# Kernel optimization log

Hardware: AMD Instinct MI355X
Metric: run time of the kernel (lower is better)

## Reference

```python
import jax, jax.numpy as jnp
import numpy as np

N_NODES = 100000
N_EDGES = 3200000
N_GRAPHS = 32
D_IN = 128
D_HID = 128
N_CLASSES = 10


def setup_inputs() -> dict:
    key = jax.random.key(0)
    ks = jax.random.split(key, 16)
    h = jax.random.normal(ks[0], (N_NODES, D_IN), dtype=jnp.float32)
    src = jax.random.randint(ks[1], (N_EDGES,), 0, N_NODES, dtype=jnp.int32)
    dst = jax.random.randint(ks[2], (N_EDGES,), 0, N_NODES, dtype=jnp.int32)
    graph_ids = jnp.sort(jax.random.randint(ks[3], (N_NODES,), 0, N_GRAPHS, dtype=jnp.int32))
    def lin(k, fi, fo):
        s = 1.0 / np.sqrt(fi)
        kw, kb = jax.random.split(k)
        W = jax.random.uniform(kw, (fi, fo), minval=-s, maxval=s, dtype=jnp.float32)
        b = jax.random.uniform(kb, (fo,), minval=-s, maxval=s, dtype=jnp.float32)
        return W, b
    W1, b1 = lin(ks[4], D_IN, D_HID)
    W2, b2 = lin(ks[5], D_HID, D_HID)
    W3, b3 = lin(ks[6], D_HID, D_HID)
    W4, b4 = lin(ks[7], D_HID, D_HID)
    Wc1, bc1 = lin(ks[8], D_HID, D_HID)
    Wc2, bc2 = lin(ks[9], D_HID, N_CLASSES)
    return {"h": h, "src": src, "dst": dst, "graph_ids": graph_ids,
            "W1": W1, "b1": b1, "W2": W2, "b2": b2, "W3": W3, "b3": b3,
            "W4": W4, "b4": b4, "Wc1": Wc1, "bc1": bc1, "Wc2": Wc2, "bc2": bc2}


def _graph_conv(h, src, dst, inv_sqrt_out, inv_sqrt_in, W, b):
    # DGL GraphConv, norm='both': D_dst^{-1/2} A D_src^{-1/2} h W + b
    m = (h * inv_sqrt_out[:, None])[src]            # [E, D] gathered messages
    agg = jax.ops.segment_sum(m, dst, num_segments=h.shape[0])  # [N, D]
    return (agg * inv_sqrt_in[:, None]) @ W + b


def reference(h, src, dst, graph_ids, W1, b1, W2, b2, W3, b3, W4, b4, Wc1, bc1, Wc2, bc2):
    n = h.shape[0]
    ones_e = jnp.ones(src.shape[0], dtype=jnp.float32)
    out_deg = jnp.clip(jax.ops.segment_sum(ones_e, src, num_segments=n), 1.0)
    in_deg = jnp.clip(jax.ops.segment_sum(ones_e, dst, num_segments=n), 1.0)
    inv_sqrt_out = jax.lax.rsqrt(out_deg)
    inv_sqrt_in = jax.lax.rsqrt(in_deg)

    x = jax.nn.relu(_graph_conv(h, src, dst, inv_sqrt_out, inv_sqrt_in, W1, b1))
    x = jax.nn.relu(_graph_conv(x, src, dst, inv_sqrt_out, inv_sqrt_in, W2, b2))
    x = jax.nn.relu(_graph_conv(x, src, dst, inv_sqrt_out, inv_sqrt_in, W3, b3))
    x = jax.nn.relu(_graph_conv(x, src, dst, inv_sqrt_out, inv_sqrt_in, W4, b4))

    # dgl.mean_nodes over batched graphs
    sums = jax.ops.segment_sum(x, graph_ids, num_segments=N_GRAPHS)     # [G, D]
    counts = jax.ops.segment_sum(jnp.ones(n, dtype=jnp.float32), graph_ids, num_segments=N_GRAPHS)
    hg = sums / jnp.clip(counts, 1.0)[:, None]

    out = jax.nn.relu(hg @ Wc1 + bc1)
    out = out @ Wc2 + bc2
    return out
```

## Files before the change

### kernel.cpp

```cpp
#include <hip/hip_runtime.h>

#define D 128
#define NG 32
#define NC 10

typedef unsigned short ushort_t;

__device__ __forceinline__ ushort_t f2bf(float x) {
  union { float f; unsigned u; } v; v.f = x;
  unsigned r = (v.u + 0x7FFF + ((v.u >> 16) & 1)) >> 16;
  return (ushort_t)r;
}
__device__ __forceinline__ float bf2f(ushort_t b) {
  union { unsigned u; float f; } v; v.u = ((unsigned)b) << 16;
  return v.f;
}

__global__ void degree_kernel(const int* __restrict__ src, const int* __restrict__ dst,
                              int* __restrict__ cout_, int* __restrict__ cursor,
                              int* __restrict__ rank, int E) {
  int i = blockIdx.x * 256 + threadIdx.x;
  int e0 = i * 4;
  if (e0 + 4 <= E) {
    int4 s = *(const int4*)(src + e0);
    int4 d_ = *(const int4*)(dst + e0);
    int r0 = atomicAdd(&cursor[d_.x], 1);
    int r1 = atomicAdd(&cursor[d_.y], 1);
    int r2 = atomicAdd(&cursor[d_.z], 1);
    int r3 = atomicAdd(&cursor[d_.w], 1);
    atomicAdd(&cout_[s.x], 1);
    atomicAdd(&cout_[s.y], 1);
    atomicAdd(&cout_[s.z], 1);
    atomicAdd(&cout_[s.w], 1);
    *(int4*)(rank + e0) = make_int4(r0, r1, r2, r3);
  } else {
    for (int e = e0; e < E; ++e) {
      rank[e] = atomicAdd(&cursor[dst[e]], 1);
      atomicAdd(&cout_[src[e]], 1);
    }
  }
}

__global__ void scan1_kernel(const int* __restrict__ cnt, int* __restrict__ bsum, int n) {
  __shared__ int sdata[256];
  int base = blockIdx.x * 1024 + threadIdx.x * 4;
  int s = 0;
#pragma unroll
  for (int j = 0; j < 4; ++j) {
    int idx = base + j;
    if (idx < n) s += cnt[idx];
  }
  sdata[threadIdx.x] = s;
  __syncthreads();
  for (int off = 128; off > 0; off >>= 1) {
    if (threadIdx.x < off) sdata[threadIdx.x] += sdata[threadIdx.x + off];
    __syncthreads();
  }
  if (threadIdx.x == 0) bsum[blockIdx.x] = sdata[0];
}

__global__ void scan2_kernel(int* __restrict__ bsum, int nb) {
  if (blockIdx.x == 0 && threadIdx.x == 0) {
    int acc = 0;
    for (int i = 0; i < nb; ++i) { int v = bsum[i]; bsum[i] = acc; acc += v; }
  }
}

__global__ void scan3_kernel(const int* __restrict__ cnt, const int* __restrict__ bsum,
                             int* __restrict__ rowptr, int n, int e_total) {
  __shared__ int ss[256];
  int t = threadIdx.x;
  int idx0 = blockIdx.x * 1024 + t * 4;
  int v[4]; int ts = 0;
#pragma unroll
  for (int j = 0; j < 4; ++j) {
    v[j] = (idx0 + j < n) ? cnt[idx0 + j] : 0;
    ts += v[j];
  }
  ss[t] = ts;
  __syncthreads();
  for (int off = 1; off < 256; off <<= 1) {
    int add = 0;
    if (t >= off) add = ss[t - off];
    __syncthreads();
    if (t >= off) ss[t] += add;
    __syncthreads();
  }
  int excl = ss[t] - ts + bsum[blockIdx.x];
#pragma unroll
  for (int j = 0; j < 4; ++j) {
    int idx = idx0 + j;
    if (idx < n) rowptr[idx] = excl;
    excl += v[j];
  }
  if (blockIdx.x == 0 && t == 0) rowptr[n] = e_total;
}

__global__ void passB_kernel(const int* __restrict__ src, const int* __restrict__ dst,
                             const int* __restrict__ rank, const int* __restrict__ rowptr,
                             int* __restrict__ csrc, int E) {
  int i = blockIdx.x * 256 + threadIdx.x;
  int e0 = i * 4;
  if (e0 + 4 <= E) {
    int4 s = *(const int4*)(src + e0);
    int4 d_ = *(const int4*)(dst + e0);
    int4 r = *(const int4*)(rank + e0);
    csrc[rowptr[d_.x] + r.x] = s.x;
    csrc[rowptr[d_.y] + r.y] = s.y;
    csrc[rowptr[d_.z] + r.z] = s.z;
    csrc[rowptr[d_.w] + r.w] = s.w;
  } else {
    for (int e = e0; e < E; ++e)
      csrc[rowptr[dst[e]] + rank[e]] = src[e];
  }
}

__global__ __launch_bounds__(256) void gemm_f32in_kernel(const float* __restrict__ A,
    const float* __restrict__ W, const int* __restrict__ cout_,
    ushort_t* __restrict__ X, int n) {
  __shared__ float As[64][132];
  int row0 = blockIdx.x * 64;
  for (int i = threadIdx.x; i < 64 * 32; i += 256) {
    int r = i >> 5, c4 = (i & 31) * 4;
    int row = row0 + r;
    float4 v = make_float4(0.f, 0.f, 0.f, 0.f);
    if (row < n) v = *(const float4*)(A + (size_t)row * D + c4);
    *(float4*)&As[r][c4] = v;
  }
  __syncthreads();
  int cg = threadIdx.x & 31, rg = threadIdx.x >> 5;
  int col = cg * 4;
  float4 acc[8];
#pragma unroll
  for (int r = 0; r < 8; ++r) acc[r] = make_float4(0.f, 0.f, 0.f, 0.f);
  for (int k = 0; k < D; k += 4) {
    float4 w0 = *(const float4*)(W + (size_t)k * D + col);
    float4 w1 = *(const float4*)(W + (size_t)(k + 1) * D + col);
    float4 w2 = *(const float4*)(W + (size_t)(k + 2) * D + col);
    float4 w3 = *(const float4*)(W + (size_t)(k + 3) * D + col);
#pragma unroll
    for (int r = 0; r < 8; ++r) {
      float4 a = *(const float4*)&As[rg * 8 + r][k];
      acc[r].x += a.x * w0.x + a.y * w1.x + a.z * w2.x + a.w * w3.x;
      acc[r].y += a.x * w0.y + a.y * w1.y + a.z * w2.y + a.w * w3.y;
      acc[r].z += a.x * w0.z + a.y * w1.z + a.z * w2.z + a.w * w3.z;
      acc[r].w += a.x * w0.w + a.y * w1.w + a.z * w2.w + a.w * w3.w;
    }
  }
#pragma unroll
  for (int r = 0; r < 8; ++r) {
    int row = row0 + rg * 8 + r;
    if (row < n) {
      float sc = rsqrtf(fmaxf((float)cout_[row], 1.f));
      ushort_t o[4] = { f2bf(acc[r].x * sc), f2bf(acc[r].y * sc),
                        f2bf(acc[r].z * sc), f2bf(acc[r].w * sc) };
      *(uint2*)(X + (size_t)row * D + col) = *(const uint2*)o;
    }
  }
}

__global__ __launch_bounds__(256) void gemm_bf16in_kernel(const ushort_t* __restrict__ A,
    const float* __restrict__ W, const int* __restrict__ cout_,
    ushort_t* __restrict__ X, int n) {
  __shared__ float As[64][132];
  int row0 = blockIdx.x * 64;
  for (int i = threadIdx.x; i < 64 * 32; i += 256) {
    int r = i >> 5, c4 = (i & 31) * 4;
    int row = row0 + r;
    float4 v = make_float4(0.f, 0.f, 0.f, 0.f);
    if (row < n) {
      ushort4 u = *(const ushort4*)(A + (size_t)row * D + c4);
      v.x = bf2f(u.x); v.y = bf2f(u.y); v.z = bf2f(u.z); v.w = bf2f(u.w);
    }
    *(float4*)&As[r][c4] = v;
  }
  __syncthreads();
  int cg = threadIdx.x & 31, rg = threadIdx.x >> 5;
  int col = cg * 4;
  float4 acc[8];
#pragma unroll
  for (int r = 0; r < 8; ++r) acc[r] = make_float4(0.f, 0.f, 0.f, 0.f);
  for (int k = 0; k < D; k += 4) {
    float4 w0 = *(const float4*)(W + (size_t)k * D + col);
    float4 w1 = *(const float4*)(W + (size_t)(k + 1) * D + col);
    float4 w2 = *(const float4*)(W + (size_t)(k + 2) * D + col);
    float4 w3 = *(const float4*)(W + (size_t)(k + 3) * D + col);
#pragma unroll
    for (int r = 0; r < 8; ++r) {
      float4 a = *(const float4*)&As[rg * 8 + r][k];
      acc[r].x += a.x * w0.x + a.y * w1.x + a.z * w2.x + a.w * w3.x;
      acc[r].y += a.x * w0.y + a.y * w1.y + a.z * w2.y + a.w * w3.y;
      acc[r].z += a.x * w0.z + a.y * w1.z + a.z * w2.z + a.w * w3.z;
      acc[r].w += a.x * w0.w + a.y * w1.w + a.z * w2.w + a.w * w3.w;
    }
  }
#pragma unroll
  for (int r = 0; r < 8; ++r) {
    int row = row0 + rg * 8 + r;
    if (row < n) {
      float sc = rsqrtf(fmaxf((float)cout_[row], 1.f));
      ushort_t o[4] = { f2bf(acc[r].x * sc), f2bf(acc[r].y * sc),
                        f2bf(acc[r].z * sc), f2bf(acc[r].w * sc) };
      *(uint2*)(X + (size_t)row * D + col) = *(const uint2*)o;
    }
  }
}

__global__ __launch_bounds__(256) void agg_relu_kernel(const ushort_t* __restrict__ x,
    const int* __restrict__ rowptr, const int* __restrict__ csrc,
    const int* __restrict__ cin_, const float* __restrict__ bias,
    ushort_t* __restrict__ y, int n) {
  int node = blockIdx.x * 4 + (threadIdx.x >> 6);
  if (node >= n) return;
  int lane = threadIdx.x & 63;
  int beg = rowptr[node], end = rowptr[node + 1];
  float ax = 0.f, ay = 0.f;
  const ushort_t* xp = x + (size_t)(lane * 2);
  int e = beg;
  for (; e + 8 <= end; e += 8) {
    int s[8];
#pragma unroll
    for (int j = 0; j < 8; ++j) s[j] = csrc[e + j];
    ushort2 u[8];
#pragma unroll
    for (int j = 0; j < 8; ++j) u[j] = *(const ushort2*)(xp + (size_t)s[j] * D);
#pragma unroll
    for (int j = 0; j < 8; ++j) { ax += bf2f(u[j].x); ay += bf2f(u[j].y); }
  }
  if (e + 4 <= end) {
    int s[4];
#pragma unroll
    for (int j = 0; j < 4; ++j) s[j] = csrc[e + j];
    ushort2 u[4];
#pragma unroll
    for (int j = 0; j < 4; ++j) u[j] = *(const ushort2*)(xp + (size_t)s[j] * D);
#pragma unroll
    for (int j = 0; j < 4; ++j) { ax += bf2f(u[j].x); ay += bf2f(u[j].y); }
    e += 4;
  }
  for (; e < end; ++e) {
    int s = csrc[e];
    ushort2 u = *(const ushort2*)(xp + (size_t)s * D);
    ax += bf2f(u.x); ay += bf2f(u.y);
  }
  float wi = rsqrtf(fmaxf((float)cin_[node], 1.f));
  float2 bb = *(const float2*)(bias + lane * 2);
  ushort_t o[2] = { f2bf(fmaxf(ax * wi + bb.x, 0.f)), f2bf(fmaxf(ay * wi + bb.y, 0.f)) };
  *(unsigned*)(y + (size_t)node * D + lane * 2) = *(const unsigned*)o;
}

__device__ int lower_bound_gid(const int* gid, int n, int g) {
  int lo = 0, hi = n;
  while (lo < hi) { int mid = (lo + hi) >> 1; if (gid[mid] < g) lo = mid + 1; else hi = mid; }
  return lo;
}

__global__ void pool_kernel(const ushort_t* __restrict__ x, const int* __restrict__ gid,
                            float* __restrict__ sums, int* __restrict__ counts, int n) {
  int g = blockIdx.x >> 3, part = blockIdx.x & 7;
  __shared__ int s_lo, s_hi;
  if (threadIdx.x == 0) {
    s_lo = lower_bound_gid(gid, n, g);
    s_hi = lower_bound_gid(gid, n, g + 1);
    if (part == 0) counts[g] = s_hi - s_lo;
  }
  __syncthreads();
  int lo = s_lo, hi = s_hi;
  int cnt = hi - lo;
  int per = (cnt + 7) >> 3;
  int a = lo + part * per;
  int bnd = min(a + per, hi);
  int t = threadIdx.x;
  float acc = 0.f;
  for (int i = a; i < bnd; ++i) acc += bf2f(x[(size_t)i * D + t]);
  atomicAdd(&sums[g * D + t], acc);
}

__global__ __launch_bounds__(128) void classifier_kernel(const float* __restrict__ sums,
    const int* __restrict__ counts, const float* __restrict__ Wc1, const float* __restrict__ bc1,
    const float* __restrict__ Wc2, const float* __restrict__ bc2, float* __restrict__ out) {
  __shared__ float hg[NG][D];
  __shared__ float hid[NG][D];
  int t = threadIdx.x;
#pragma unroll
  for (int g = 0; g < NG; ++g)
    hg[g][t] = sums[g * D + t] / fmaxf((float)counts[g], 1.f);
  __syncthreads();
  float acc[NG];
#pragma unroll
  for (int g = 0; g < NG; ++g) acc[g] = bc1[t];
  for (int k = 0; k < D; ++k) {
    float w = Wc1[k * D + t];
#pragma unroll
    for (int g = 0; g < NG; ++g) acc[g] += hg[g][k] * w;
  }
#pragma unroll
  for (int g = 0; g < NG; ++g) hid[g][t] = fmaxf(acc[g], 0.f);
  __syncthreads();
  for (int idx = t; idx < NG * NC; idx += 128) {
    int g = idx / NC, c = idx % NC;
    float a = bc2[c];
    for (int j = 0; j < D; ++j) a += hid[g][j] * Wc2[j * NC + c];
    out[idx] = a;
  }
}

extern "C" void kernel_launch(void* const* d_in, const int* in_sizes, int n_in,
                              void* d_out, int out_size, void* d_ws, size_t ws_size,
                              hipStream_t stream) {
  const float* h   = (const float*)d_in[0];
  const int* src   = (const int*)d_in[1];
  const int* dst   = (const int*)d_in[2];
  const int* gid   = (const int*)d_in[3];
  const float* W1  = (const float*)d_in[4];
  const float* b1  = (const float*)d_in[5];
  const float* W2  = (const float*)d_in[6];
  const float* b2  = (const float*)d_in[7];
  const float* W3  = (const float*)d_in[8];
  const float* b3  = (const float*)d_in[9];
  const float* W4  = (const float*)d_in[10];
  const float* b4  = (const float*)d_in[11];
  const float* Wc1 = (const float*)d_in[12];
  const float* bc1 = (const float*)d_in[13];
  const float* Wc2 = (const float*)d_in[14];
  const float* bc2 = (const float*)d_in[15];
  float* out = (float*)d_out;

  const int N = in_sizes[3];
  const int E = in_sizes[1];

  char* ws = (char*)d_ws;
  size_t off = 0;
  auto alloc = [&](size_t bytes) -> char* {
    char* p = ws + off;
    off = (off + bytes + 255) & ~(size_t)255;
    return p;
  };

  int* cnts     = (int*)alloc((size_t)2 * N * 4);
  int* cout_    = cnts;
  int* cursor   = cnts + N;
  int* rowptr   = (int*)alloc((size_t)(N + 1) * 4);
  int* bsum     = (int*)alloc(1024);
  int* csrc     = (int*)alloc((size_t)E * 4);
  ushort_t* Xb  = (ushort_t*)alloc((size_t)N * D * 2);
  ushort_t* Yb  = (ushort_t*)alloc((size_t)N * D * 2);
  float* sums   = (float*)alloc((size_t)(NG * D + NG) * 4);
  int* counts   = (int*)(sums + NG * D);
  int* rank     = (int*)Yb;

  hipMemsetAsync(cnts, 0, (size_t)2 * N * 4, stream);
  hipMemsetAsync(sums, 0, (size_t)(NG * D + NG) * 4, stream);

  int gE4 = (E / 4 + 255) / 256 + 1;
  int nb = (N + 1023) / 1024;
  int gAgg  = (N + 3) / 4;
  int gGemm = (N + 63) / 64;

  degree_kernel<<<gE4, 256, 0, stream>>>(src, dst, cout_, cursor, rank, E);
  scan1_kernel<<<nb, 256, 0, stream>>>(cursor, bsum, N);
  scan2_kernel<<<1, 64, 0, stream>>>(bsum, nb);
  scan3_kernel<<<nb, 256, 0, stream>>>(cursor, bsum, rowptr, N, E);
  passB_kernel<<<gE4, 256, 0, stream>>>(src, dst, rank, rowptr, csrc, E);

  gemm_f32in_kernel<<<gGemm, 256, 0, stream>>>(h, W1, cout_, Xb, N);
  agg_relu_kernel<<<gAgg, 256, 0, stream>>>(Xb, rowptr, csrc, cursor, b1, Yb, N);
  gemm_bf16in_kernel<<<gGemm, 256, 0, stream>>>(Yb, W2, cout_, Xb, N);
  agg_relu_kernel<<<gAgg, 256, 0, stream>>>(Xb, rowptr, csrc, cursor, b2, Yb, N);
  gemm_bf16in_kernel<<<gGemm, 256, 0, stream>>>(Yb, W3, cout_, Xb, N);
  agg_relu_kernel<<<gAgg, 256, 0, stream>>>(Xb, rowptr, csrc, cursor, b3, Yb, N);
  gemm_bf16in_kernel<<<gGemm, 256, 0, stream>>>(Yb, W4, cout_, Xb, N);
  agg_relu_kernel<<<gAgg, 256, 0, stream>>>(Xb, rowptr, csrc, cursor, b4, Yb, N);

  pool_kernel<<<NG * 8, 128, 0, stream>>>(Yb, gid, sums, counts, N);
  classifier_kernel<<<1, 128, 0, stream>>>(sums, counts, Wc1, bc1, Wc2, bc2, out);
}
```

Before: 1.141 ms.

## Use bf16 MFMA for layer GEMMs and replicate out-degree counters

```diff
diff --git a/kernel.cpp b/kernel.cpp
--- a/kernel.cpp
+++ b/kernel.cpp
@@ -5,6 +5,8 @@
 #define NC 10
 
 typedef unsigned short ushort_t;
+typedef __attribute__((ext_vector_type(8))) short short8v;
+typedef __attribute__((ext_vector_type(4))) float float4v;
 
 __device__ __forceinline__ ushort_t f2bf(float x) {
   union { float f; unsigned u; } v; v.f = x;
@@ -17,8 +19,9 @@
 }
 
 __global__ void degree_kernel(const int* __restrict__ src, const int* __restrict__ dst,
-                              int* __restrict__ cout_, int* __restrict__ cursor,
-                              int* __restrict__ rank, int E) {
+                              int* __restrict__ cout_r, int* __restrict__ cursor,
+                              int* __restrict__ rank, int E, int n) {
+  int* co = cout_r + (size_t)(blockIdx.x & 3) * n;
   int i = blockIdx.x * 256 + threadIdx.x;
   int e0 = i * 4;
   if (e0 + 4 <= E) {
@@ -28,17 +31,23 @@
     int r1 = atomicAdd(&cursor[d_.y], 1);
     int r2 = atomicAdd(&cursor[d_.z], 1);
     int r3 = atomicAdd(&cursor[d_.w], 1);
-    atomicAdd(&cout_[s.x], 1);
-    atomicAdd(&cout_[s.y], 1);
-    atomicAdd(&cout_[s.z], 1);
-    atomicAdd(&cout_[s.w], 1);
+    atomicAdd(&co[s.x], 1);
+    atomicAdd(&co[s.y], 1);
+    atomicAdd(&co[s.z], 1);
+    atomicAdd(&co[s.w], 1);
     *(int4*)(rank + e0) = make_int4(r0, r1, r2, r3);
   } else {
     for (int e = e0; e < E; ++e) {
       rank[e] = atomicAdd(&cursor[dst[e]], 1);
-      atomicAdd(&cout_[src[e]], 1);
+      atomicAdd(&co[src[e]], 1);
     }
   }
+}
+
+__global__ void sumdeg_kernel(const int* __restrict__ cout_r, int* __restrict__ cout_, int n) {
+  int i = blockIdx.x * 256 + threadIdx.x;
+  if (i < n)
+    cout_[i] = cout_r[i] + cout_r[n + i] + cout_r[2 * (size_t)n + i] + cout_r[3 * (size_t)n + i];
 }
 
 __global__ void scan1_kernel(const int* __restrict__ cnt, int* __restrict__ bsum, int n) {
@@ -115,93 +124,77 @@
   }
 }
 
-__global__ __launch_bounds__(256) void gemm_f32in_kernel(const float* __restrict__ A,
-    const float* __restrict__ W, const int* __restrict__ cout_,
+__global__ void cvt_h_kernel(const float* __restrict__ h, ushort_t* __restrict__ hb, long total) {
+  long i4 = ((long)blockIdx.x * 256 + threadIdx.x) * 4;
+  if (i4 + 4 <= total) {
+    float4 v = *(const float4*)(h + i4);
+    ushort_t o[4] = { f2bf(v.x), f2bf(v.y), f2bf(v.z), f2bf(v.w) };
+    *(uint2*)(hb + i4) = *(const uint2*)o;
+  } else {
+    for (long i = i4; i < total; ++i) hb[i] = f2bf(h[i]);
+  }
+}
+
+__global__ void cvt_w_kernel(const float* __restrict__ W1, const float* __restrict__ W2,
+                             const float* __restrict__ W3, const float* __restrict__ W4,
+                             ushort_t* __restrict__ Wt) {
+  const float* Ws[4] = { W1, W2, W3, W4 };
+  const float* W = Ws[blockIdx.x];
+  ushort_t* o = Wt + (size_t)blockIdx.x * D * D;
+  for (int idx = threadIdx.x; idx < D * D; idx += 256) {
+    int c = idx >> 7, k = idx & 127;
+    o[c * D + k] = f2bf(W[k * D + c]);
+  }
+}
+
+__global__ __launch_bounds__(256) void gemm_mfma_kernel(const ushort_t* __restrict__ A,
+    const ushort_t* __restrict__ Wt, const int* __restrict__ cout_,
     ushort_t* __restrict__ X, int n) {
-  __shared__ float As[64][132];
-  int row0 = blockIdx.x * 64;
-  for (int i = threadIdx.x; i < 64 * 32; i += 256) {
-    int r = i >> 5, c4 = (i & 31) * 4;
-    int row = row0 + r;
-    float4 v = make_float4(0.f, 0.f, 0.f, 0.f);
-    if (row < n) v = *(const float4*)(A + (size_t)row * D + c4);
-    *(float4*)&As[r][c4] = v;
-  }
-  __syncthreads();
-  int cg = threadIdx.x & 31, rg = threadIdx.x >> 5;
-  int col = cg * 4;
-  float4 acc[8];
-#pragma unroll
-  for (int r = 0; r < 8; ++r) acc[r] = make_float4(0.f, 0.f, 0.f, 0.f);
-  for (int k = 0; k < D; k += 4) {
-    float4 w0 = *(const float4*)(W + (size_t)k * D + col);
-    float4 w1 = *(const float4*)(W + (size_t)(k + 1) * D + col);
-    float4 w2 = *(const float4*)(W + (size_t)(k + 2) * D + col);
-    float4 w3 = *(const float4*)(W + (size_t)(k + 3) * D + col);
-#pragma unroll
-    for (int r = 0; r < 8; ++r) {
-      float4 a = *(const float4*)&As[rg * 8 + r][k];
-      acc[r].x += a.x * w0.x + a.y * w1.x + a.z * w2.x + a.w * w3.x;
-      acc[r].y += a.x * w0.y + a.y * w1.y + a.z * w2.y + a.w * w3.y;
-      acc[r].z += a.x * w0.z + a.y * w1.z + a.z * w2.z + a.w * w3.z;
-      acc[r].w += a.x * w0.w + a.y * w1.w + a.z * w2.w + a.w * w3.w;
+  int wave = threadIdx.x >> 6;
+  int lane = threadIdx.x & 63;
+  int g = lane >> 4;
+  int lr = lane & 15;
+  int rowbase = blockIdx.x * 64 + wave * 16;
+  int arow = rowbase + lr;
+  int arow_c = arow < n ? arow : (n - 1);
+  const ushort_t* Ap = A + (size_t)arow_c * D + g * 8;
+
+  short8v afrag[4];
+#pragma unroll
+  for (int ks = 0; ks < 4; ++ks)
+    afrag[ks] = *(const short8v*)(Ap + ks * 32);
+
+  float4v acc[8];
+#pragma unroll
+  for (int ct = 0; ct < 8; ++ct)
+#pragma unroll
+    for (int r = 0; r < 4; ++r) acc[ct][r] = 0.f;
+
+#pragma unroll
+  for (int ct = 0; ct < 8; ++ct) {
+    const ushort_t* bp = Wt + (size_t)(ct * 16 + lr) * D + g * 8;
+#pragma unroll
+    for (int ks = 0; ks < 4; ++ks) {
+      short8v bfrag = *(const short8v*)(bp + ks * 32);
+      acc[ct] = __builtin_amdgcn_mfma_f32_16x16x32_bf16(afrag[ks], bfrag, acc[ct], 0, 0, 0);
     }
   }
-#pragma unroll
-  for (int r = 0; r < 8; ++r) {
-    int row = row0 + rg * 8 + r;
-    if (row < n) {
-      float sc = rsqrtf(fmaxf((float)cout_[row], 1.f));
-      ushort_t o[4] = { f2bf(acc[r].x * sc), f2bf(acc[r].y * sc),
-                        f2bf(acc[r].z * sc), f2bf(acc[r].w * sc) };
-      *(uint2*)(X + (size_t)row * D + col) = *(const uint2*)o;
-    }
-  }
-}
-
-__global__ __launch_bounds__(256) void gemm_bf16in_kernel(const ushort_t* __restrict__ A,
-    const float* __restrict__ W, const int* __restrict__ cout_,
-    ushort_t* __restrict__ X, int n) {
-  __shared__ float As[64][132];
-  int row0 = blockIdx.x * 64;
-  for (int i = threadIdx.x; i < 64 * 32; i += 256) {
-    int r = i >> 5, c4 = (i & 31) * 4;
-    int row = row0 + r;
-    float4 v = make_float4(0.f, 0.f, 0.f, 0.f);
-    if (row < n) {
-      ushort4 u = *(const ushort4*)(A + (size_t)row * D + c4);
-      v.x = bf2f(u.x); v.y = bf2f(u.y); v.z = bf2f(u.z); v.w = bf2f(u.w);
-    }
-    *(float4*)&As[r][c4] = v;
-  }
-  __syncthreads();
-  int cg = threadIdx.x & 31, rg = threadIdx.x >> 5;
-  int col = cg * 4;
-  float4 acc[8];
-#pragma unroll
-  for (int r = 0; r < 8; ++r) acc[r] = make_float4(0.f, 0.f, 0.f, 0.f);
-  for (int k = 0; k < D; k += 4) {
-    float4 w0 = *(const float4*)(W + (size_t)k * D + col);
-    float4 w1 = *(const float4*)(W + (size_t)(k + 1) * D + col);
-    float4 w2 = *(const float4*)(W + (size_t)(k + 2) * D + col);
-    float4 w3 = *(const float4*)(W + (size_t)(k + 3) * D + col);
-#pragma unroll
-    for (int r = 0; r < 8; ++r) {
-      float4 a = *(const float4*)&As[rg * 8 + r][k];
-      acc[r].x += a.x * w0.x + a.y * w1.x + a.z * w2.x + a.w * w3.x;
-      acc[r].y += a.x * w0.y + a.y * w1.y + a.z * w2.y + a.w * w3.y;
-      acc[r].z += a.x * w0.z + a.y * w1.z + a.z * w2.z + a.w * w3.z;
-      acc[r].w += a.x * w0.w + a.y * w1.w + a.z * w2.w + a.w * w3.w;
-    }
-  }
-#pragma unroll
-  for (int r = 0; r < 8; ++r) {
-    int row = row0 + rg * 8 + r;
-    if (row < n) {
-      float sc = rsqrtf(fmaxf((float)cout_[row], 1.f));
-      ushort_t o[4] = { f2bf(acc[r].x * sc), f2bf(acc[r].y * sc),
-                        f2bf(acc[r].z * sc), f2bf(acc[r].w * sc) };
-      *(uint2*)(X + (size_t)row * D + col) = *(const uint2*)o;
+
+  float scv[4];
+  bool rok[4];
+#pragma unroll
+  for (int r = 0; r < 4; ++r) {
+    int grow = rowbase + g * 4 + r;
+    rok[r] = grow < n;
+    int gc = rok[r] ? grow : (n - 1);
+    scv[r] = rsqrtf(fmaxf((float)cout_[gc], 1.f));
+  }
+#pragma unroll
+  for (int ct = 0; ct < 8; ++ct) {
+#pragma unroll
+    for (int r = 0; r < 4; ++r) {
+      int grow = rowbase + g * 4 + r;
+      if (rok[r]) X[(size_t)grow * D + ct * 16 + lr] = f2bf(acc[ct][r] * scv[r]);
     }
   }
 }
@@ -337,39 +330,49 @@
     return p;
   };
 
-  int* cnts     = (int*)alloc((size_t)2 * N * 4);
-  int* cout_    = cnts;
-  int* cursor   = cnts + N;
+  int* cnts     = (int*)alloc((size_t)5 * N * 4);
+  int* cout_r   = cnts;
+  int* cursor   = cnts + (size_t)4 * N;
+  int* cout_    = (int*)alloc((size_t)N * 4);
   int* rowptr   = (int*)alloc((size_t)(N + 1) * 4);
   int* bsum     = (int*)alloc(1024);
   int* csrc     = (int*)alloc((size_t)E * 4);
+  ushort_t* Wt  = (ushort_t*)alloc((size_t)4 * D * D * 2);
   ushort_t* Xb  = (ushort_t*)alloc((size_t)N * D * 2);
   ushort_t* Yb  = (ushort_t*)alloc((size_t)N * D * 2);
   float* sums   = (float*)alloc((size_t)(NG * D + NG) * 4);
   int* counts   = (int*)(sums + NG * D);
   int* rank     = (int*)Yb;
-
-  hipMemsetAsync(cnts, 0, (size_t)2 * N * 4, stream);
+  ushort_t* Hb  = Yb;
+
+  hipMemsetAsync(cnts, 0, (size_t)5 * N * 4, stream);
   hipMemsetAsync(sums, 0, (size_t)(NG * D + NG) * 4, stream);
 
   int gE4 = (E / 4 + 255) / 256 + 1;
-  int nb = (N + 1023) / 1024;
+  int gN  = (N + 255) / 256;
+  int nb  = (N + 1023) / 1024;
   int gAgg  = (N + 3) / 4;
   int gGemm = (N + 63) / 64;
-
-  degree_kernel<<<gE4, 256, 0, stream>>>(src, dst, cout_, cursor, rank, E);
+  long totalH = (long)N * D;
+  int gCvt = (int)((totalH / 4 + 255) / 256) + 1;
+
+  degree_kernel<<<gE4, 256, 0, stream>>>(src, dst, cout_r, cursor, rank, E, N);
+  sumdeg_kernel<<<gN, 256, 0, stream>>>(cout_r, cout_, N);
   scan1_kernel<<<nb, 256, 0, stream>>>(cursor, bsum, N);
   scan2_kernel<<<1, 64, 0, stream>>>(bsum, nb);
   scan3_kernel<<<nb, 256, 0, stream>>>(cursor, bsum, rowptr, N, E);
   passB_kernel<<<gE4, 256, 0, stream>>>(src, dst, rank, rowptr, csrc, E);
 
-  gemm_f32in_kernel<<<gGemm, 256, 0, stream>>>(h, W1, cout_, Xb, N);
+  cvt_w_kernel<<<4, 256, 0, stream>>>(W1, W2, W3, W4, Wt);
+  cvt_h_kernel<<<gCvt, 256, 0, stream>>>(h, Hb, totalH);
+
+  gemm_mfma_kernel<<<gGemm, 256, 0, stream>>>(Hb, Wt, cout_, Xb, N);
   agg_relu_kernel<<<gAgg, 256, 0, stream>>>(Xb, rowptr, csrc, cursor, b1, Yb, N);
-  gemm_bf16in_kernel<<<gGemm, 256, 0, stream>>>(Yb, W2, cout_, Xb, N);
+  gemm_mfma_kernel<<<gGemm, 256, 0, stream>>>(Yb, Wt + (size_t)1 * D * D, cout_, Xb, N);
   agg_relu_kernel<<<gAgg, 256, 0, stream>>>(Xb, rowptr, csrc, cursor, b2, Yb, N);
-  gemm_bf16in_kernel<<<gGemm, 256, 0, stream>>>(Yb, W3, cout_, Xb, N);
+  gemm_mfma_kernel<<<gGemm, 256, 0, stream>>>(Yb, Wt + (size_t)2 * D * D, cout_, Xb, N);
   agg_relu_kernel<<<gAgg, 256, 0, stream>>>(Xb, rowptr, csrc, cursor, b3, Yb, N);
-  gemm_bf16in_kernel<<<gGemm, 256, 0, stream>>>(Yb, W4, cout_, Xb, N);
+  gemm_mfma_kernel<<<gGemm, 256, 0, stream>>>(Yb, Wt + (size_t)3 * D * D, cout_, Xb, N);
   agg_relu_kernel<<<gAgg, 256, 0, stream>>>(Xb, rowptr, csrc, cursor, b4, Yb, N);
 
   pool_kernel<<<NG * 8, 128, 0, stream>>>(Yb, gid, sums, counts, N);
```

Result: faster. 1.076 ms (-5.8%).
